# Performance work log

Measured on AMD Instinct MI355X. Metric: run time of the kernel, lower is better.

Reference implementation:

```python
import jax, jax.numpy as jnp
import numpy as np

N_VOXELS = 2_000_000
NUM_CLUSTERS = 20_000


def setup_inputs() -> dict:
    key = jax.random.key(0)
    k1, k2 = jax.random.split(key)
    data = jax.random.normal(k1, (N_VOXELS, 6), dtype=jnp.float32)
    clusts = jax.random.randint(k2, (N_VOXELS,), 0, NUM_CLUSTERS, dtype=jnp.int32)
    return {"data": data, "clusts": clusts}


def reference(data, clusts):
    # data: [N, 6]; clusts: [N] segment ids in [0, NUM_CLUSTERS)
    C = NUM_CLUSTERS
    voxels = data[:, :3]  # [N, 3]
    seg = clusts

    counts = jax.ops.segment_sum(jnp.ones((voxels.shape[0],), voxels.dtype), seg, num_segments=C)  # [C]
    center = jax.ops.segment_sum(voxels, seg, num_segments=C) / counts[:, None]  # [C, 3]

    xc = voxels - center[seg]  # centered coords, [N, 3]
    # per-cluster scatter matrix A = x^T x, [C, 3, 3]
    A = jax.ops.segment_sum(xc[:, :, None] * xc[:, None, :], seg, num_segments=C)

    # eigh returns ascending eigenvalues, same convention as torch.symeig
    w, v = jnp.linalg.eigh(A)  # w: [C, 3], v: [C, 3, 3]
    w2 = w[:, 2]
    dirwt = 1.0 - w[:, 1] / w2  # [C]
    B = A / w2[:, None, None]  # normalized scatter matrix, [C, 3, 3]
    v0 = v[:, :, 2]  # principal axis, [C, 3]

    # direction disambiguation: sc = dot(x0, ||x - x0 v0||)
    v0n = v0[seg]  # [N, 3]
    x0 = jnp.einsum('nd,nd->n', xc, v0n)  # projection onto principal axis
    xp0 = xc - x0[:, None] * v0n  # residual off-axis component
    np0 = jnp.linalg.norm(xp0, axis=1)
    sc = jax.ops.segment_sum(x0 * np0, seg, num_segments=C)  # [C]

    v0 = jnp.where(sc[:, None] < 0, -v0, v0) * dirwt[:, None]

    # features: center(3) | B flat(9) | v0(3) | size(1) -> [C, 16]
    return jnp.concatenate([center, B.reshape(C, 9), v0, counts[:, None]], axis=1)
```

## Files before the change

### kernel.cpp

```cpp
#include <hip/hip_runtime.h>
#include <hip/hip_bf16.h>
#include <math.h>

#define NVOX    2000000
#define NCLUST  20000
#define NBUCK   625
#define CLB     32
#define CAPB    4096
#define VPB     4096
#define FS_TB   1024
#define P2TB    512
#define HCLB    16
#define CAP_CL  192

struct ClustOut {
    float cx, cy, cz;
    float B[9];
    float vx, vy, vz;
    float dirwt;
    float n;
};

__device__ inline ClustOut eig_from_moments(float a0, float a1, float a2, float a3,
                                            float a4, float a5, float a6, float a7,
                                            float a8, float a9) {
    ClustOut o;
    float n  = a0;
    float inv = (n > 0.0f) ? (1.0f / n) : 0.0f;
    float cx = a1 * inv, cy = a2 * inv, cz = a3 * inv;
    float A00 = a4 - a1 * cx;
    float A01 = a5 - a1 * cy;
    float A02 = a6 - a1 * cz;
    float A11 = a7 - a2 * cy;
    float A12 = a8 - a2 * cz;
    float A22 = a9 - a3 * cz;

    float q = (A00 + A11 + A22) * (1.0f / 3.0f);
    float b00 = A00 - q, b11 = A11 - q, b22 = A22 - q;
    float p2 = b00 * b00 + b11 * b11 + b22 * b22
             + 2.0f * (A01 * A01 + A02 * A02 + A12 * A12);
    float p = sqrtf(p2 * (1.0f / 6.0f));
    float w0, w1, w2;
    if (p > 1e-30f) {
        float invp = 1.0f / p;
        float c00 = b00 * invp, c11 = b11 * invp, c22 = b22 * invp;
        float c01 = A01 * invp, c02 = A02 * invp, c12 = A12 * invp;
        float det = c00 * (c11 * c22 - c12 * c12)
                  - c01 * (c01 * c22 - c12 * c02)
                  + c02 * (c01 * c12 - c11 * c02);
        float r = 0.5f * det;
        r = fminf(1.0f, fmaxf(-1.0f, r));
        float phi = acosf(r) * (1.0f / 3.0f);
        w2 = q + 2.0f * p * cosf(phi);
        w0 = q + 2.0f * p * cosf(phi + 2.0943951023931953f);
        w1 = 3.0f * q - w2 - w0;
    } else {
        w0 = w1 = w2 = q;
    }

    float invw2 = (w2 != 0.0f) ? (1.0f / w2) : 0.0f;
    o.dirwt = 1.0f - w1 * invw2;

    float M0[9] = { A00 - w0, A01, A02,
                    A01, A11 - w0, A12,
                    A02, A12, A22 - w0 };
    float M1[9] = { A00 - w1, A01, A02,
                    A01, A11 - w1, A12,
                    A02, A12, A22 - w1 };
    float P[9];
#pragma unroll
    for (int i = 0; i < 3; ++i)
#pragma unroll
        for (int j = 0; j < 3; ++j)
            P[i * 3 + j] = M0[i * 3 + 0] * M1[0 * 3 + j]
                         + M0[i * 3 + 1] * M1[1 * 3 + j]
                         + M0[i * 3 + 2] * M1[2 * 3 + j];
    float n0 = P[0] * P[0] + P[3] * P[3] + P[6] * P[6];
    float n1 = P[1] * P[1] + P[4] * P[4] + P[7] * P[7];
    float n2 = P[2] * P[2] + P[5] * P[5] + P[8] * P[8];
    float vx, vy, vz, nn;
    if (n0 >= n1 && n0 >= n2)      { vx = P[0]; vy = P[3]; vz = P[6]; nn = n0; }
    else if (n1 >= n2)             { vx = P[1]; vy = P[4]; vz = P[7]; nn = n1; }
    else                           { vx = P[2]; vy = P[5]; vz = P[8]; nn = n2; }
    if (nn > 1e-30f) {
        float s = 1.0f / sqrtf(nn);
        vx *= s; vy *= s; vz *= s;
    } else {
        vx = vy = vz = 0.0f;
    }
    o.cx = cx; o.cy = cy; o.cz = cz;
    o.vx = vx; o.vy = vy; o.vz = vz;
    o.n = n;
    o.B[0] = A00 * invw2; o.B[1] = A01 * invw2; o.B[2] = A02 * invw2;
    o.B[3] = A01 * invw2; o.B[4] = A11 * invw2; o.B[5] = A12 * invw2;
    o.B[6] = A02 * invw2; o.B[7] = A12 * invw2; o.B[8] = A22 * invw2;
    return o;
}

__device__ inline void write_row(float* out, int c, const ClustOut& o, float score) {
    float f = (score < 0.0f) ? -o.dirwt : o.dirwt;
    float4* o4 = reinterpret_cast<float4*>(out + (size_t)c * 16);
    o4[0] = make_float4(o.cx, o.cy, o.cz, o.B[0]);
    o4[1] = make_float4(o.B[1], o.B[2], o.B[3], o.B[4]);
    o4[2] = make_float4(o.B[5], o.B[6], o.B[7], o.B[8]);
    o4[3] = make_float4(o.vx * f, o.vy * f, o.vz * f, o.n);
}


__global__ __launch_bounds__(FS_TB) void k_fscatter(const float* __restrict__ data,
                                                    const int* __restrict__ clusts,
                                                    unsigned int* __restrict__ gcnt,
                                                    float4* __restrict__ sv4, int n) {
    __shared__ unsigned int h[NBUCK];
    __shared__ unsigned int live[NBUCK];
    int b = blockIdx.x;
    for (int w = threadIdx.x; w < NBUCK; w += FS_TB) h[w] = 0;
    __syncthreads();

    int s = b * VPB;
    float4 r0, r1, r2, r3;
    int c0 = -1, c1 = -1, c2 = -1, c3 = -1;
    int i0 = s + threadIdx.x, i1 = i0 + FS_TB, i2 = i1 + FS_TB, i3 = i2 + FS_TB;
    if (i0 < n) {
        const float* d = data + (size_t)i0 * 6;
        float2 xy = *reinterpret_cast<const float2*>(d);
        c0 = clusts[i0];
        r0 = make_float4(xy.x, xy.y, d[2], __int_as_float(c0));
        atomicAdd(&h[c0 >> 5], 1u);
    }
    if (i1 < n) {
        const float* d = data + (size_t)i1 * 6;
        float2 xy = *reinterpret_cast<const float2*>(d);
        c1 = clusts[i1];
        r1 = make_float4(xy.x, xy.y, d[2], __int_as_float(c1));
        atomicAdd(&h[c1 >> 5], 1u);
    }
    if (i2 < n) {
        const float* d = data + (size_t)i2 * 6;
        float2 xy = *reinterpret_cast<const float2*>(d);
        c2 = clusts[i2];
        r2 = make_float4(xy.x, xy.y, d[2], __int_as_float(c2));
        atomicAdd(&h[c2 >> 5], 1u);
    }
    if (i3 < n) {
        const float* d = data + (size_t)i3 * 6;
        float2 xy = *reinterpret_cast<const float2*>(d);
        c3 = clusts[i3];
        r3 = make_float4(xy.x, xy.y, d[2], __int_as_float(c3));
        atomicAdd(&h[c3 >> 5], 1u);
    }
    __syncthreads();

    for (int w = threadIdx.x; w < NBUCK; w += FS_TB) {
        unsigned int cnt = h[w];
        unsigned int base = cnt ? atomicAdd(&gcnt[w], cnt) : 0u;
        live[w] = (unsigned int)w * CAPB + base;
    }
    __syncthreads();

    if (c0 >= 0) {
        unsigned int j = atomicAdd(&live[c0 >> 5], 1u);
        if (j < (unsigned int)((c0 >> 5) + 1) * CAPB) sv4[j] = r0;
    }
    if (c1 >= 0) {
        unsigned int j = atomicAdd(&live[c1 >> 5], 1u);
        if (j < (unsigned int)((c1 >> 5) + 1) * CAPB) sv4[j] = r1;
    }
    if (c2 >= 0) {
        unsigned int j = atomicAdd(&live[c2 >> 5], 1u);
        if (j < (unsigned int)((c2 >> 5) + 1) * CAPB) sv4[j] = r2;
    }
    if (c3 >= 0) {
        unsigned int j = atomicAdd(&live[c3 >> 5], 1u);
        if (j < (unsigned int)((c3 >> 5) + 1) * CAPB) sv4[j] = r3;
    }
}

__global__ __launch_bounds__(P2TB) void k_bpass2(const float4* __restrict__ sv4,
                                                 const unsigned int* __restrict__ gcnt,
                                                 float* __restrict__ out) {
    __shared__ float4 vox[HCLB][CAP_CL];
    __shared__ unsigned int hc[HCLB];
    int blk = blockIdx.x;
    int bkt = blk >> 1, half = blk & 1;
    unsigned int seg0 = (unsigned int)bkt * CAPB;
    unsigned int cnt = min(gcnt[bkt], (unsigned int)CAPB);
    int t = threadIdx.x, wv = t >> 6, lane = t & 63;

    if (t < HCLB) hc[t] = 0;
    __syncthreads();

#pragma unroll
    for (int k = 0; k < CAPB / P2TB; ++k) {
        unsigned int i = (unsigned int)t + (unsigned int)k * P2TB;
        if (i < cnt) {
            float4 v = sv4[seg0 + i];
            int id = __float_as_int(v.w) - bkt * CLB;
            if ((id >> 4) == half) {
                int lc = id & 15;
                unsigned int r = atomicAdd(&hc[lc], 1u);
                if (r < CAP_CL) vox[lc][r] = v;
            }
        }
    }
    __syncthreads();

#pragma unroll
    for (int k = 0; k < 2; ++k) {
        int lc = wv * 2 + k;
        unsigned int e = min(hc[lc], (unsigned int)CAP_CL);
        float a0 = 0, a1 = 0, a2 = 0, a3 = 0, a4 = 0,
              a5 = 0, a6 = 0, a7 = 0, a8 = 0, a9 = 0;
        for (unsigned int j = lane; j < e; j += 64) {
            float4 v = vox[lc][j];
            float x = v.x, y = v.y, z = v.z;
            a0 += 1.0f;
            a1 += x; a2 += y; a3 += z;
            a4 += x * x; a5 += x * y; a6 += x * z;
            a7 += y * y; a8 += y * z; a9 += z * z;
        }
#pragma unroll
        for (int m = 32; m; m >>= 1) {
            a0 += __shfl_xor(a0, m); a1 += __shfl_xor(a1, m);
            a2 += __shfl_xor(a2, m); a3 += __shfl_xor(a3, m);
            a4 += __shfl_xor(a4, m); a5 += __shfl_xor(a5, m);
            a6 += __shfl_xor(a6, m); a7 += __shfl_xor(a7, m);
            a8 += __shfl_xor(a8, m); a9 += __shfl_xor(a9, m);
        }
        ClustOut o = eig_from_moments(a0, a1, a2, a3, a4, a5, a6, a7, a8, a9);
        float sum = 0.0f;
        for (unsigned int j = lane; j < e; j += 64) {
            float4 v = vox[lc][j];
            float xcx = v.x - o.cx, xcy = v.y - o.cy, xcz = v.z - o.cz;
            float x0 = xcx * o.vx + xcy * o.vy + xcz * o.vz;
            float px = xcx - x0 * o.vx;
            float py = xcy - x0 * o.vy;
            float pz = xcz - x0 * o.vz;
            sum += x0 * sqrtf(px * px + py * py + pz * pz);
        }
#pragma unroll
        for (int m = 32; m; m >>= 1) sum += __shfl_xor(sum, m);
        if (lane == 0) write_row(out, bkt * CLB + half * HCLB + lc, o, sum);
    }
}

__global__ __launch_bounds__(256) void k_accum(const float* __restrict__ data,
                                               const int* __restrict__ clusts,
                                               float* __restrict__ mom, int n) {
    int i = blockIdx.x * blockDim.x + threadIdx.x;
    if (i >= n) return;
    const float* d = data + (size_t)i * 6;
    float2 xy = *reinterpret_cast<const float2*>(d);
    float x = xy.x, y = xy.y, z = d[2];
    int c = clusts[i];
    float* m = mom + (size_t)c * 10;
    atomicAdd(m + 0, 1.0f);
    atomicAdd(m + 1, x);
    atomicAdd(m + 2, y);
    atomicAdd(m + 3, z);
    atomicAdd(m + 4, x * x);
    atomicAdd(m + 5, x * y);
    atomicAdd(m + 6, x * z);
    atomicAdd(m + 7, y * y);
    atomicAdd(m + 8, y * z);
    atomicAdd(m + 9, z * z);
}

__global__ __launch_bounds__(256) void k_eigen(const float* __restrict__ mom,
                                               float* __restrict__ out,
                                               float* __restrict__ dirwt_ws, int C) {
    int c = blockIdx.x * blockDim.x + threadIdx.x;
    if (c >= C) return;
    const float* m = mom + (size_t)c * 10;
    ClustOut o = eig_from_moments(m[0], m[1], m[2], m[3], m[4],
                                  m[5], m[6], m[7], m[8], m[9]);
    float* p = out + (size_t)c * 16;
    p[0] = o.cx; p[1] = o.cy; p[2] = o.cz;
#pragma unroll
    for (int k = 0; k < 9; ++k) p[3 + k] = o.B[k];
    p[12] = o.vx; p[13] = o.vy; p[14] = o.vz;
    p[15] = o.n;
    dirwt_ws[c] = o.dirwt;
}

__global__ __launch_bounds__(256) void k_score(const float* __restrict__ data,
                                               const int* __restrict__ clusts,
                                               const float* __restrict__ out,
                                               float* __restrict__ sc, int n) {
    int i = blockIdx.x * blockDim.x + threadIdx.x;
    if (i >= n) return;
    const float* d = data + (size_t)i * 6;
    float2 xy = *reinterpret_cast<const float2*>(d);
    float x = xy.x, y = xy.y, z = d[2];
    int c = clusts[i];
    const float* o = out + (size_t)c * 16;
    float xcx = x - o[0], xcy = y - o[1], xcz = z - o[2];
    float vx = o[12], vy = o[13], vz = o[14];
    float x0 = xcx * vx + xcy * vy + xcz * vz;
    float px = xcx - x0 * vx;
    float py = xcy - x0 * vy;
    float pz = xcz - x0 * vz;
    atomicAdd(&sc[c], x0 * sqrtf(px * px + py * py + pz * pz));
}

__global__ __launch_bounds__(256) void k_final(const float* __restrict__ sc,
                                               const float* __restrict__ dirwt_ws,
                                               float* __restrict__ out, int C) {
    int c = blockIdx.x * blockDim.x + threadIdx.x;
    if (c >= C) return;
    float f = dirwt_ws[c];
    if (sc[c] < 0.0f) f = -f;
    float* o = out + (size_t)c * 16;
    o[12] *= f; o[13] *= f; o[14] *= f;
}

extern "C" void kernel_launch(void* const* d_in, const int* in_sizes, int n_in,
                              void* d_out, int out_size, void* d_ws, size_t ws_size,
                              hipStream_t stream) {
    const float* data  = (const float*)d_in[0];
    const int* clusts  = (const int*)d_in[1];
    float* out         = (float*)d_out;

    const int C = NCLUST;
    const int n = in_sizes[1];
    const int NB = (n + VPB - 1) / VPB;

    size_t off = 0;
    auto alloc = [&](size_t bytes) {
        size_t o = off;
        off += (bytes + 255) & ~(size_t)255;
        return o;
    };
    size_t o_gcnt = alloc((size_t)NBUCK * sizeof(unsigned int));
    size_t o_sv4  = alloc((size_t)NBUCK * CAPB * sizeof(float4));
    size_t needed = off;

    char* ws = (char*)d_ws;

    if (ws_size >= needed) {
        unsigned int* gcnt = (unsigned int*)(ws + o_gcnt);
        float4*       sv4  = (float4*)(ws + o_sv4);

        hipMemsetAsync(gcnt, 0, (size_t)NBUCK * sizeof(unsigned int), stream);
        k_fscatter<<<NB, FS_TB, 0, stream>>>(data, clusts, gcnt, sv4, n);
        k_bpass2<<<NBUCK * 2, P2TB, 0, stream>>>(sv4, gcnt, out);
    } else {
        float* mom   = (float*)d_ws;
        float* sc    = mom + (size_t)10 * C;
        float* dirwt = sc + C;
        hipMemsetAsync(d_ws, 0, (size_t)11 * C * sizeof(float), stream);
        const int gbv = (n + 255) / 256;
        const int gbc = (C + 255) / 256;
        k_accum<<<gbv, 256, 0, stream>>>(data, clusts, mom, n);
        k_eigen<<<gbc, 256, 0, stream>>>(mom, out, dirwt, C);
        k_score<<<gbv, 256, 0, stream>>>(data, clusts, out, sc, n);
        k_final<<<gbc, 256, 0, stream>>>(sc, dirwt, out, C);
    }
}
```

Before: 135.4 us.

## Stage voxels in LDS by region before scattering and halve bucket width

The scatter kernel now computes a block-local prefix scan over 16-cluster regions, writes its voxels into shared memory sorted by region, and then emits them to global memory in that order so neighbouring threads write neighbouring addresses. Bucket width drops from 32 to 16 clusters, so the second pass reads only its own region's voxels instead of reading a 32-cluster bucket twice and discarding half. Histogram counters are packed two per word to save shared memory. The cost is 64KB of LDS per block, which lowers occupancy, plus an extra scan and sync phase.

```diff
diff --git a/kernel.cpp b/kernel.cpp
--- a/kernel.cpp
+++ b/kernel.cpp
@@ -4,13 +4,13 @@
 
 #define NVOX    2000000
 #define NCLUST  20000
-#define NBUCK   625
-#define CLB     32
-#define CAPB    4096
+#define NREG    1250
+#define HREG    (NREG/2)
+#define CLR     16
+#define CAPR    2048
 #define VPB     4096
 #define FS_TB   1024
 #define P2TB    512
-#define HCLB    16
 #define CAP_CL  192
 
 struct ClustOut {
@@ -111,97 +111,118 @@
                                                     const int* __restrict__ clusts,
                                                     unsigned int* __restrict__ gcnt,
                                                     float4* __restrict__ sv4, int n) {
-    __shared__ unsigned int h[NBUCK];
-    __shared__ unsigned int live[NBUCK];
+    __shared__ unsigned int h[HREG];
+    __shared__ unsigned int scn[HREG];
+    __shared__ unsigned int live[NREG];
+    __shared__ unsigned int dsto[NREG];
+    __shared__ float4 vox[VPB];
+
+    int t = threadIdx.x;
     int b = blockIdx.x;
-    for (int w = threadIdx.x; w < NBUCK; w += FS_TB) h[w] = 0;
-    __syncthreads();
-
     int s = b * VPB;
+    int btotal = min(n - s, VPB);
+
+    for (int w = t; w < HREG; w += FS_TB) h[w] = 0;
+    __syncthreads();
+
     float4 r0, r1, r2, r3;
-    int c0 = -1, c1 = -1, c2 = -1, c3 = -1;
-    int i0 = s + threadIdx.x, i1 = i0 + FS_TB, i2 = i1 + FS_TB, i3 = i2 + FS_TB;
-    if (i0 < n) {
-        const float* d = data + (size_t)i0 * 6;
+    int g0 = -1, g1 = -1, g2 = -1, g3 = -1;
+    int i0 = t, i1 = i0 + FS_TB, i2 = i1 + FS_TB, i3 = i2 + FS_TB;
+    if (i0 < btotal) {
+        const float* d = data + (size_t)(s + i0) * 6;
         float2 xy = *reinterpret_cast<const float2*>(d);
-        c0 = clusts[i0];
-        r0 = make_float4(xy.x, xy.y, d[2], __int_as_float(c0));
-        atomicAdd(&h[c0 >> 5], 1u);
-    }
-    if (i1 < n) {
-        const float* d = data + (size_t)i1 * 6;
+        int c = clusts[s + i0];
+        r0 = make_float4(xy.x, xy.y, d[2], __int_as_float(c));
+        g0 = c >> 4;
+        atomicAdd(&h[g0 >> 1], 1u << ((g0 & 1) * 16));
+    }
+    if (i1 < btotal) {
+        const float* d = data + (size_t)(s + i1) * 6;
         float2 xy = *reinterpret_cast<const float2*>(d);
-        c1 = clusts[i1];
-        r1 = make_float4(xy.x, xy.y, d[2], __int_as_float(c1));
-        atomicAdd(&h[c1 >> 5], 1u);
-    }
-    if (i2 < n) {
-        const float* d = data + (size_t)i2 * 6;
+        int c = clusts[s + i1];
+        r1 = make_float4(xy.x, xy.y, d[2], __int_as_float(c));
+        g1 = c >> 4;
+        atomicAdd(&h[g1 >> 1], 1u << ((g1 & 1) * 16));
+    }
+    if (i2 < btotal) {
+        const float* d = data + (size_t)(s + i2) * 6;
         float2 xy = *reinterpret_cast<const float2*>(d);
-        c2 = clusts[i2];
-        r2 = make_float4(xy.x, xy.y, d[2], __int_as_float(c2));
-        atomicAdd(&h[c2 >> 5], 1u);
-    }
-    if (i3 < n) {
-        const float* d = data + (size_t)i3 * 6;
+        int c = clusts[s + i2];
+        r2 = make_float4(xy.x, xy.y, d[2], __int_as_float(c));
+        g2 = c >> 4;
+        atomicAdd(&h[g2 >> 1], 1u << ((g2 & 1) * 16));
+    }
+    if (i3 < btotal) {
+        const float* d = data + (size_t)(s + i3) * 6;
         float2 xy = *reinterpret_cast<const float2*>(d);
-        c3 = clusts[i3];
-        r3 = make_float4(xy.x, xy.y, d[2], __int_as_float(c3));
-        atomicAdd(&h[c3 >> 5], 1u);
-    }
-    __syncthreads();
-
-    for (int w = threadIdx.x; w < NBUCK; w += FS_TB) {
-        unsigned int cnt = h[w];
-        unsigned int base = cnt ? atomicAdd(&gcnt[w], cnt) : 0u;
-        live[w] = (unsigned int)w * CAPB + base;
-    }
-    __syncthreads();
-
-    if (c0 >= 0) {
-        unsigned int j = atomicAdd(&live[c0 >> 5], 1u);
-        if (j < (unsigned int)((c0 >> 5) + 1) * CAPB) sv4[j] = r0;
-    }
-    if (c1 >= 0) {
-        unsigned int j = atomicAdd(&live[c1 >> 5], 1u);
-        if (j < (unsigned int)((c1 >> 5) + 1) * CAPB) sv4[j] = r1;
-    }
-    if (c2 >= 0) {
-        unsigned int j = atomicAdd(&live[c2 >> 5], 1u);
-        if (j < (unsigned int)((c2 >> 5) + 1) * CAPB) sv4[j] = r2;
-    }
-    if (c3 >= 0) {
-        unsigned int j = atomicAdd(&live[c3 >> 5], 1u);
-        if (j < (unsigned int)((c3 >> 5) + 1) * CAPB) sv4[j] = r3;
+        int c = clusts[s + i3];
+        r3 = make_float4(xy.x, xy.y, d[2], __int_as_float(c));
+        g3 = c >> 4;
+        atomicAdd(&h[g3 >> 1], 1u << ((g3 & 1) * 16));
+    }
+    __syncthreads();
+
+    if (t < HREG) {
+        unsigned int v = h[t];
+        scn[t] = (v & 0xFFFFu) + (v >> 16);
+    }
+    __syncthreads();
+    for (int off = 1; off < HREG; off <<= 1) {
+        unsigned int v = (t >= off && t < HREG) ? scn[t - off] : 0u;
+        __syncthreads();
+        if (t < HREG) scn[t] += v;
+        __syncthreads();
+    }
+
+    for (int w = t; w < NREG; w += FS_TB) {
+        int wd = w >> 1;
+        unsigned int packed = h[wd];
+        unsigned int lo = packed & 0xFFFFu;
+        unsigned int exclw = (wd == 0) ? 0u : scn[wd - 1];
+        unsigned int base = exclw + ((w & 1) ? lo : 0u);
+        unsigned int cntw = (w & 1) ? (packed >> 16) : lo;
+        unsigned int gbase = cntw ? atomicAdd(&gcnt[w], cntw) : 0u;
+        live[w] = base;
+        dsto[w] = (unsigned int)w * CAPR + gbase - base;
+    }
+    __syncthreads();
+
+    if (g0 >= 0) vox[atomicAdd(&live[g0], 1u)] = r0;
+    if (g1 >= 0) vox[atomicAdd(&live[g1], 1u)] = r1;
+    if (g2 >= 0) vox[atomicAdd(&live[g2], 1u)] = r2;
+    if (g3 >= 0) vox[atomicAdd(&live[g3], 1u)] = r3;
+    __syncthreads();
+
+#pragma unroll
+    for (int k = 0; k < VPB / FS_TB; ++k) {
+        int i = t + k * FS_TB;
+        if (i < btotal) {
+            float4 v = vox[i];
+            int w = __float_as_int(v.w) >> 4;
+            unsigned int j = dsto[w] + (unsigned int)i;
+            if (j < (unsigned int)(w + 1) * CAPR) sv4[j] = v;
+        }
     }
 }
 
 __global__ __launch_bounds__(P2TB) void k_bpass2(const float4* __restrict__ sv4,
                                                  const unsigned int* __restrict__ gcnt,
                                                  float* __restrict__ out) {
-    __shared__ float4 vox[HCLB][CAP_CL];
-    __shared__ unsigned int hc[HCLB];
-    int blk = blockIdx.x;
-    int bkt = blk >> 1, half = blk & 1;
-    unsigned int seg0 = (unsigned int)bkt * CAPB;
-    unsigned int cnt = min(gcnt[bkt], (unsigned int)CAPB);
+    __shared__ float4 vox[CLR][CAP_CL];
+    __shared__ unsigned int hc[CLR];
+    int rid = blockIdx.x;
+    unsigned int seg0 = (unsigned int)rid * CAPR;
+    unsigned int cnt = min(gcnt[rid], (unsigned int)CAPR);
     int t = threadIdx.x, wv = t >> 6, lane = t & 63;
 
-    if (t < HCLB) hc[t] = 0;
-    __syncthreads();
-
-#pragma unroll
-    for (int k = 0; k < CAPB / P2TB; ++k) {
-        unsigned int i = (unsigned int)t + (unsigned int)k * P2TB;
-        if (i < cnt) {
-            float4 v = sv4[seg0 + i];
-            int id = __float_as_int(v.w) - bkt * CLB;
-            if ((id >> 4) == half) {
-                int lc = id & 15;
-                unsigned int r = atomicAdd(&hc[lc], 1u);
-                if (r < CAP_CL) vox[lc][r] = v;
-            }
-        }
+    if (t < CLR) hc[t] = 0;
+    __syncthreads();
+
+    for (unsigned int i = t; i < cnt; i += P2TB) {
+        float4 v = sv4[seg0 + i];
+        int lc = __float_as_int(v.w) & 15;
+        unsigned int r = atomicAdd(&hc[lc], 1u);
+        if (r < CAP_CL) vox[lc][r] = v;
     }
     __syncthreads();
 
@@ -240,7 +261,7 @@
         }
 #pragma unroll
         for (int m = 32; m; m >>= 1) sum += __shfl_xor(sum, m);
-        if (lane == 0) write_row(out, bkt * CLB + half * HCLB + lc, o, sum);
+        if (lane == 0) write_row(out, rid * CLR + lc, o, sum);
     }
 }
 
@@ -331,8 +352,8 @@
         off += (bytes + 255) & ~(size_t)255;
         return o;
     };
-    size_t o_gcnt = alloc((size_t)NBUCK * sizeof(unsigned int));
-    size_t o_sv4  = alloc((size_t)NBUCK * CAPB * sizeof(float4));
+    size_t o_gcnt = alloc((size_t)NREG * sizeof(unsigned int));
+    size_t o_sv4  = alloc((size_t)NREG * CAPR * sizeof(float4));
     size_t needed = off;
 
     char* ws = (char*)d_ws;
@@ -341,9 +362,9 @@
         unsigned int* gcnt = (unsigned int*)(ws + o_gcnt);
         float4*       sv4  = (float4*)(ws + o_sv4);
 
-        hipMemsetAsync(gcnt, 0, (size_t)NBUCK * sizeof(unsigned int), stream);
+        hipMemsetAsync(gcnt, 0, (size_t)NREG * sizeof(unsigned int), stream);
         k_fscatter<<<NB, FS_TB, 0, stream>>>(data, clusts, gcnt, sv4, n);
-        k_bpass2<<<NBUCK * 2, P2TB, 0, stream>>>(sv4, gcnt, out);
+        k_bpass2<<<NREG, P2TB, 0, stream>>>(sv4, gcnt, out);
     } else {
         float* mom   = (float*)d_ws;
         float* sc    = mom + (size_t)10 * C;
```

Result: no change. 134.3 us (-0.8%).
